# Kernel optimization log

Measured on AMD Instinct MI355X. Metric: run time of the kernel, lower is better.

## Reference

```python
import jax, jax.numpy as jnp
import numpy as np

MAX_RADIUS = 0.9
TEMP = 0.1

def _to_poincare(x, W, b):
    # Linear + Tanh, then rescale into Poincare ball of radius 0.9
    h = jnp.tanh(x @ W.T + b)
    norm = jnp.clip(jnp.linalg.norm(h, axis=-1, keepdims=True), 1e-8, None)
    scale = jnp.where(norm > MAX_RADIUS, MAX_RADIUS / norm, jnp.ones_like(norm))
    return h * scale

def setup_inputs() -> dict:
    key = jax.random.key(0)
    kq, kw, kb, km, ko = jax.random.split(key, 5)
    B, N, D = 2048, 100000, 128
    return {
        "query": jax.random.normal(kq, (B, D), dtype=jnp.float32),
        "W": jax.random.normal(kw, (D, D), dtype=jnp.float32) * (1.0 / np.sqrt(D)),
        "b": jax.random.normal(kb, (D,), dtype=jnp.float32) * 0.01,
        "mem_emb": jax.random.normal(km, (N, D), dtype=jnp.float32),
        "mem_out": jax.random.normal(ko, (N, D), dtype=jnp.float32),
        "k": 16,
    }

def reference(query, W, b, mem_emb, mem_out, k):
    q = _to_poincare(query, W, b)          # [B, D]
    m = _to_poincare(mem_emb, W, b)        # [N, D]
    # Euclidean cdist via the GEMM form: ||q||^2 + ||m||^2 - 2 q.m
    q2 = jnp.sum(q * q, axis=-1, keepdims=True)           # [B, 1]
    m2 = jnp.sum(m * m, axis=-1)                          # [N]
    d2 = q2 + m2[None, :] - 2.0 * (q @ m.T)               # [B, N]
    dists = jnp.sqrt(jnp.maximum(d2, 1e-12))
    # k smallest distances
    neg_top, top_idx = jax.lax.top_k(-dists, k)           # [B, k]
    top_dists = -neg_top
    weights = jax.nn.softmax(-top_dists / TEMP, axis=-1)  # [B, k]
    outcomes = mem_out[top_idx]                           # [B, k, D]
    return weights, outcomes
```

## Files before the change

### kernel.cpp

```cpp
#include <hip/hip_runtime.h>
#include <hip/hip_bf16.h>
#include <math.h>

#define DIM 128
#define QB 128
#define MB 64
#define NSPLIT 32
#define KSEL 16
#define KOWN 4
#define RESCORE 32
#define IDXMASK 0x1FFFu
#define KEYMASK 0xFFFFE000u
#define M2MAX 3200

using bf16x8 = __attribute__((ext_vector_type(8))) short;
using f32x4  = __attribute__((ext_vector_type(4))) float;

__device__ inline unsigned short f2bf(float f) {
  __hip_bfloat16 h = __float2bfloat16(f);
  return __builtin_bit_cast(unsigned short, h);
}
__device__ inline unsigned uminu(unsigned a, unsigned b) {
  return __builtin_elementwise_min(a, b);
}
__device__ inline unsigned umaxu(unsigned a, unsigned b) {
  return __builtin_elementwise_max(a, b);
}
__device__ inline unsigned long long umin64(unsigned long long a,
                                            unsigned long long b) {
  return __builtin_elementwise_min(a, b);
}

__device__ inline f32x4 mfma16(bf16x8 a, bf16x8 b, f32x4 c) {
  return __builtin_amdgcn_mfma_f32_16x16x32_bf16(a, b, c, 0, 0, 0);
}

__device__ inline void gload_lds16(const void* g, void* l) {
  __builtin_amdgcn_global_load_lds(
      (const __attribute__((address_space(1))) void*)g,
      (__attribute__((address_space(3))) void*)l, 16, 0, 0);
}

__device__ inline void ins4(unsigned (&ks)[KOWN], unsigned c) {
  #pragma unroll
  for (int i = 0; i < KOWN; ++i) {
    const unsigned lo = uminu(c, ks[i]);
    c = umaxu(c, ks[i]);
    ks[i] = lo;
  }
}

__global__ __launch_bounds__(512) void poincare2_k(
    const float* __restrict__ Xm, int Rm,
    const float* __restrict__ Xq, int Rq,
    const float* __restrict__ W, const float* __restrict__ bias,
    float* __restrict__ Pm, float* __restrict__ Pm2,
    float* __restrict__ Pm2s, int npadm,
    unsigned short* __restrict__ Pmbf,
    float* __restrict__ Pq, float* __restrict__ Pq2, int nbm)
{
  __shared__ float Xl[128 * DIM];
  __shared__ float nrm[128 * 8];
  __shared__ float norm2l[128];

  const int t  = threadIdx.x;
  const int l  = t & 63;
  const int wv_ = t >> 6;
  const int jw = __builtin_amdgcn_readfirstlane(wv_ * 16);

  const bool ismem = (int)blockIdx.x < nbm;
  const float* X = ismem ? Xm : Xq;
  const int    R = ismem ? Rm : Rq;
  float*       P  = ismem ? Pm  : Pq;
  float*       P2 = ismem ? Pm2 : Pq2;
  unsigned short* Pbf = ismem ? Pmbf : nullptr;
  const int rbase = (ismem ? blockIdx.x : (blockIdx.x - nbm)) * 128;

  for (int i = t; i < 128 * 32; i += 512) {
    const int r = i >> 5, c = i & 31;
    int row = rbase + r; if (row > R - 1) row = R - 1;
    const float4 v = *(const float4*)&X[(size_t)row * DIM + c * 4];
    *(float4*)&Xl[r * DIM + ((c ^ ((r >> 1) & 7)) << 2)] = v;
  }

  float acc0[16], acc1[16];
  #pragma unroll
  for (int u = 0; u < 16; ++u) {
    const float b = bias[jw + u];
    acc0[u] = b; acc1[u] = b;
  }
  __syncthreads();

  const float* Wb = W + jw * DIM;
  const int x0 = (2 * l) * DIM;
  const int x1 = x0 + DIM;
  #pragma unroll 2
  for (int k4 = 0; k4 < 32; ++k4) {
    const int ch = (k4 ^ (l & 7)) << 2;
    const float4 xv0 = *(const float4*)&Xl[x0 + ch];
    const float4 xv1 = *(const float4*)&Xl[x1 + ch];
    #pragma unroll
    for (int u = 0; u < 16; ++u) {
      const float4 wvv = *(const float4*)(Wb + u * DIM + k4 * 4);
      acc0[u] = fmaf(xv0.x, wvv.x, acc0[u]);
      acc0[u] = fmaf(xv0.y, wvv.y, acc0[u]);
      acc0[u] = fmaf(xv0.z, wvv.z, acc0[u]);
      acc0[u] = fmaf(xv0.w, wvv.w, acc0[u]);
      acc1[u] = fmaf(xv1.x, wvv.x, acc1[u]);
      acc1[u] = fmaf(xv1.y, wvv.y, acc1[u]);
      acc1[u] = fmaf(xv1.z, wvv.z, acc1[u]);
      acc1[u] = fmaf(xv1.w, wvv.w, acc1[u]);
    }
  }

  float pn0 = 0.f, pn1 = 0.f;
  #pragma unroll
  for (int u = 0; u < 16; ++u) {
    acc0[u] = tanhf(acc0[u]); pn0 = fmaf(acc0[u], acc0[u], pn0);
    acc1[u] = tanhf(acc1[u]); pn1 = fmaf(acc1[u], acc1[u], pn1);
  }
  __syncthreads();
  {
    const int cb = jw >> 2;
    #pragma unroll
    for (int u4 = 0; u4 < 4; ++u4) {
      const int pos = ((cb + u4) ^ (l & 7)) << 2;
      *(float4*)&Xl[x0 + pos] = make_float4(acc0[u4*4], acc0[u4*4+1],
                                            acc0[u4*4+2], acc0[u4*4+3]);
      *(float4*)&Xl[x1 + pos] = make_float4(acc1[u4*4], acc1[u4*4+1],
                                            acc1[u4*4+2], acc1[u4*4+3]);
    }
    nrm[(2 * l) * 8 + wv_]     = pn0;
    nrm[(2 * l + 1) * 8 + wv_] = pn1;
  }
  __syncthreads();
  if (t < 128) {
    float s = 0.f;
    #pragma unroll
    for (int j = 0; j < 8; ++j) s += nrm[t * 8 + j];
    norm2l[t] = s;
    const int row = rbase + t;
    if (row < R) {
      const float nm = sqrtf(s);
      const float sc = (nm > 0.9f) ? (0.9f / nm) : 1.0f;
      const float p2v = s * sc * sc;
      P2[row] = p2v;
      if (ismem) Pm2s[row] = fmaf(0.5f, p2v, 1.0f);
    } else if (ismem && row < npadm) {
      Pm2s[row] = __int_as_float(0x7f800000);
    }
  }
  __syncthreads();

  const int cg = t & 15, rg = t >> 4;
  #pragma unroll
  for (int v = 0; v < 4; ++v) {
    const int r = rg + 32 * v;
    const int row = rbase + r;
    if (row < R) {
      const float n2 = norm2l[r];
      const float nm = sqrtf(n2);
      const float sc = (nm > 0.9f) ? (0.9f / nm) : 1.0f;
      const int sw = (r >> 1) & 7;
      const float4 h0 = *(const float4*)&Xl[r * DIM + (((2*cg)   ^ sw) << 2)];
      const float4 h1 = *(const float4*)&Xl[r * DIM + (((2*cg+1) ^ sw) << 2)];
      float o[8] = {h0.x*sc, h0.y*sc, h0.z*sc, h0.w*sc,
                    h1.x*sc, h1.y*sc, h1.z*sc, h1.w*sc};
      *(float4*)&P[(size_t)row * DIM + cg * 8]     = make_float4(o[0], o[1], o[2], o[3]);
      *(float4*)&P[(size_t)row * DIM + cg * 8 + 4] = make_float4(o[4], o[5], o[6], o[7]);
      if (Pbf) {
        uint4 pb;
        pb.x = (unsigned)f2bf(o[0]) | ((unsigned)f2bf(o[1]) << 16);
        pb.y = (unsigned)f2bf(o[2]) | ((unsigned)f2bf(o[3]) << 16);
        pb.z = (unsigned)f2bf(o[4]) | ((unsigned)f2bf(o[5]) << 16);
        pb.w = (unsigned)f2bf(o[6]) | ((unsigned)f2bf(o[7]) << 16);
        *(uint4*)&Pmbf[(size_t)row * DIM + ((cg ^ (row & 15)) << 3)] = pb;
      }
    }
  }
}

template<bool USEBF>
__global__ __launch_bounds__(512, 2) void score_topk_k(
    const float* __restrict__ Pq,
    const float* __restrict__ Pm, const float* __restrict__ Pm2s,
    const unsigned short* __restrict__ Pmbf,
    int N, int splitlen, unsigned* __restrict__ splitTop)
{
  __shared__ __align__(16) unsigned short Ml[3][MB * DIM];
  __shared__ float m2all[M2MAX];

  const int t = threadIdx.x;
  const int lane = t & 63;
  const int w = t >> 6, wr = w >> 1, wc = w & 1;
  const int split = blockIdx.x;
  const int qbase = blockIdx.y * QB;
  const int mlo = split * splitlen;
  const int mhi = min(mlo + splitlen, N);
  const int ntiles = (mhi - mlo + MB - 1) / MB;

  bf16x8 qf[2][4];
  #pragma unroll
  for (int s = 0; s < 2; ++s) {
    const int qrow = qbase + wr * 32 + s * 16 + (lane & 15);
    #pragma unroll
    for (int ks = 0; ks < 4; ++ks) {
      const float* src = &Pq[(size_t)qrow * DIM + ks * 32 + (lane >> 4) * 8];
      float4 lo = *(const float4*)src;
      float4 hi = *(const float4*)(src + 4);
      bf16x8 v;
      v[0] = (short)f2bf(-lo.x); v[1] = (short)f2bf(-lo.y);
      v[2] = (short)f2bf(-lo.z); v[3] = (short)f2bf(-lo.w);
      v[4] = (short)f2bf(-hi.x); v[5] = (short)f2bf(-hi.y);
      v[6] = (short)f2bf(-hi.z); v[7] = (short)f2bf(-hi.w);
      qf[s][ks] = v;
    }
  }

  for (int i = t; i < splitlen; i += 512) m2all[i] = Pm2s[mlo + i];

  const size_t soff0 = (size_t)(w * 8 + (lane >> 4)) * DIM + ((lane & 15) << 3);
  const size_t soff1 = soff0 + 4 * DIM;

  auto stageU = [&](int tilei, int buf) {
    const unsigned short* b = Pmbf + (size_t)(mlo + tilei * MB) * DIM;
    gload_lds16(b + soff0, &Ml[buf][(w * 8) * DIM]);
    gload_lds16(b + soff1, &Ml[buf][(w * 8 + 4) * DIM]);
  };
  uint4 sv0, sv1;
  auto stageF_load = [&](int tilei) {
    const int fr = t >> 3, fe = t & 7;
    const float* src = Pm + (size_t)(mlo + tilei * MB + fr) * DIM + fe * 16;
    float4 a0 = *(const float4*)(src + 0);
    float4 a1 = *(const float4*)(src + 4);
    float4 a2 = *(const float4*)(src + 8);
    float4 a3 = *(const float4*)(src + 12);
    sv0.x = (unsigned)f2bf(a0.x) | ((unsigned)f2bf(a0.y) << 16);
    sv0.y = (unsigned)f2bf(a0.z) | ((unsigned)f2bf(a0.w) << 16);
    sv0.z = (unsigned)f2bf(a1.x) | ((unsigned)f2bf(a1.y) << 16);
    sv0.w = (unsigned)f2bf(a1.z) | ((unsigned)f2bf(a1.w) << 16);
    sv1.x = (unsigned)f2bf(a2.x) | ((unsigned)f2bf(a2.y) << 16);
    sv1.y = (unsigned)f2bf(a2.z) | ((unsigned)f2bf(a2.w) << 16);
    sv1.z = (unsigned)f2bf(a3.x) | ((unsigned)f2bf(a3.y) << 16);
    sv1.w = (unsigned)f2bf(a3.z) | ((unsigned)f2bf(a3.w) << 16);
  };
  auto stageF_write = [&](int buf) {
    const int fr = t >> 3, fe = t & 7;
    char* base = (char*)&Ml[buf][0] + fr * 256;
    *(uint4*)(base + (((2 * fe)     ^ (fr & 15)) << 4)) = sv0;
    *(uint4*)(base + (((2 * fe + 1) ^ (fr & 15)) << 4)) = sv1;
  };

  unsigned keys[2][4][KOWN];
  #pragma unroll
  for (int s = 0; s < 2; ++s)
    #pragma unroll
    for (int r = 0; r < 4; ++r)
      #pragma unroll
      for (int i = 0; i < KOWN; ++i) keys[s][r][i] = 0xFFFFFFFFu;

  const int mcol = wc * 32 + (lane & 15);
  const int rowA = mcol, rowB = mcol + 16;

  auto compute = [&](int tile, const unsigned short* cur) {
    const float ca = m2all[tile * MB + mcol];
    const float cb = m2all[tile * MB + mcol + 16];
    f32x4 a00 = (f32x4){ca, ca, ca, ca};
    f32x4 a01 = (f32x4){cb, cb, cb, cb};
    f32x4 a10 = (f32x4){ca, ca, ca, ca};
    f32x4 a11 = (f32x4){cb, cb, cb, cb};
    __builtin_amdgcn_s_setprio(1);
    #pragma unroll
    for (int ks = 0; ks < 4; ++ks) {
      const int kb = ks * 64 + (lane >> 4) * 16;
      bf16x8 bfrA = *(const bf16x8*)((const char*)cur + rowA * 256 +
                                     (kb ^ ((rowA & 15) << 4)));
      bf16x8 bfrB = *(const bf16x8*)((const char*)cur + rowB * 256 +
                                     (kb ^ ((rowB & 15) << 4)));
      a00 = mfma16(qf[0][ks], bfrA, a00);
      a01 = mfma16(qf[0][ks], bfrB, a01);
      a10 = mfma16(qf[1][ks], bfrA, a10);
      a11 = mfma16(qf[1][ks], bfrB, a11);
    }
    __builtin_amdgcn_s_setprio(0);
    const unsigned idx0 = (unsigned)(tile * MB + mcol);
    #pragma unroll
    for (int r = 0; r < 4; ++r) {
      ins4(keys[0][r], (__float_as_uint(a00[r]) & KEYMASK) | idx0);
      ins4(keys[0][r], (__float_as_uint(a01[r]) & KEYMASK) | (idx0 + 16));
      ins4(keys[1][r], (__float_as_uint(a10[r]) & KEYMASK) | idx0);
      ins4(keys[1][r], (__float_as_uint(a11[r]) & KEYMASK) | (idx0 + 16));
    }
  };

  if constexpr (USEBF) {
    __syncthreads();
    stageU(0, 0);
    if (ntiles > 1) stageU(1, 1);
    int cur = 0;
    for (int i = 0; i < ntiles; ++i) {
      if (i < ntiles - 1) asm volatile("s_waitcnt vmcnt(2)" ::: "memory");
      else                asm volatile("s_waitcnt vmcnt(0)" ::: "memory");
      __builtin_amdgcn_s_barrier();
      __builtin_amdgcn_sched_barrier(0);
      int nb = cur + 2; if (nb >= 3) nb -= 3;
      if (i + 2 < ntiles) stageU(i + 2, nb);
      compute(i, &Ml[cur][0]);
      cur = (cur + 1 == 3) ? 0 : cur + 1;
    }
  } else {
    stageF_load(0);
    stageF_write(0);
    __syncthreads();
    for (int i = 0; i < ntiles; ++i) {
      const int cur = i & 1;
      const bool more = (i + 1 < ntiles);
      if (more) stageF_load(i + 1);
      compute(i, &Ml[cur][0]);
      __syncthreads();
      if (more) stageF_write(cur ^ 1);
      __syncthreads();
    }
  }

  unsigned* mb = (unsigned*)&Ml[0][0];
  __syncthreads();
  #pragma unroll
  for (int s = 0; s < 2; ++s)
    #pragma unroll
    for (int r = 0; r < 4; ++r) {
      unsigned k0 = keys[s][r][0], k1 = keys[s][r][1];
      unsigned k2 = keys[s][r][2], k3 = keys[s][r][3];
      unsigned out = 0xFFFFFFFFu;
      for (int round = 0; round < 8; ++round) {
        unsigned g = k0;
        g = uminu(g, __shfl_xor(g, 1, 16));
        g = uminu(g, __shfl_xor(g, 2, 16));
        g = uminu(g, __shfl_xor(g, 4, 16));
        g = uminu(g, __shfl_xor(g, 8, 16));
        const bool mine = (k0 == g);
        k0 = mine ? k1 : k0;
        k1 = mine ? k2 : k1;
        k2 = mine ? k3 : k2;
        k3 = mine ? 0xFFFFFFFFu : k3;
        if ((lane & 15) == round) out = g;
      }
      const int lq = wr * 32 + s * 16 + (lane >> 4) * 4 + r;
      if ((lane & 15) < 8) mb[lq * 16 + wc * 8 + (lane & 15)] = out;
    }
  __syncthreads();
  if (wc == 0 && lane < 32) {
    const int lq = wr * 32 + lane;
    unsigned s8[8];
    #pragma unroll
    for (int i = 0; i < 8; ++i) s8[i] = 0xFFFFFFFFu;
    const unsigned* src = mb + lq * 16;
    #pragma unroll
    for (int i = 0; i < 16; ++i) {
      unsigned c = src[i];
      #pragma unroll
      for (int j = 0; j < 8; ++j) {
        const unsigned lo = uminu(c, s8[j]);
        c = umaxu(c, s8[j]);
        s8[j] = lo;
      }
    }
    unsigned* dst = &splitTop[((size_t)(qbase + lq) * NSPLIT + split) * 8];
    *(uint4*)dst       = make_uint4(s8[0], s8[1], s8[2], s8[3]);
    *((uint4*)dst + 1) = make_uint4(s8[4], s8[5], s8[6], s8[7]);
  }
}

__global__ __launch_bounds__(256) void finalize_k(
    const unsigned* __restrict__ splitTop,
    const float* __restrict__ Pq, const float* __restrict__ Pq2,
    const float* __restrict__ Pm, const float* __restrict__ Pm2,
    const float* __restrict__ memOut, int N, int splitlen,
    float* __restrict__ outW, float* __restrict__ outO)
{
  const int wv   = threadIdx.x >> 6;
  const int lane = threadIdx.x & 63;
  const int q = blockIdx.x * 4 + wv;

  __shared__ unsigned      sKey[4][RESCORE];
  __shared__ unsigned char sSrc[4][RESCORE];
  __shared__ unsigned long long sKeyx[4][RESCORE];
  __shared__ unsigned long long sSel[4][KSEL];
  __shared__ float sEl[4][KSEL];

  {
    unsigned a[8];
    if (lane < NSPLIT) {
      const unsigned* gp = splitTop + (size_t)q * (NSPLIT * 8) + lane * 8;
      uint4 lo = *(const uint4*)gp;
      uint4 hi = *(const uint4*)(gp + 4);
      a[0] = lo.x; a[1] = lo.y; a[2] = lo.z; a[3] = lo.w;
      a[4] = hi.x; a[5] = hi.y; a[6] = hi.z; a[7] = hi.w;
    } else {
      #pragma unroll
      for (int i = 0; i < 8; ++i) a[i] = 0xFFFFFFFFu;
    }
    for (int r = 0; r < RESCORE; ++r) {
      unsigned g = a[0];
      g = uminu(g, __shfl_xor(g, 1));
      g = uminu(g, __shfl_xor(g, 2));
      g = uminu(g, __shfl_xor(g, 4));
      g = uminu(g, __shfl_xor(g, 8));
      g = uminu(g, __shfl_xor(g, 16));
      g = uminu(g, __shfl_xor(g, 32));
      unsigned long long mask = __ballot(a[0] == g);
      const int fl = __ffsll((unsigned long long)mask) - 1;
      if (lane == fl) {
        #pragma unroll
        for (int i = 0; i < 7; ++i) a[i] = a[i + 1];
        a[7] = 0xFFFFFFFFu;
      }
      if (lane == 0) { sKey[wv][r] = g; sSrc[wv][r] = (unsigned char)fl; }
    }
  }

  #pragma unroll
  for (int p = 0; p < 4; ++p) {
    const int g8 = p * 8 + (lane >> 3), e = lane & 7;
    const int gidx = (int)sSrc[wv][g8] * splitlen + (int)(sKey[wv][g8] & IDXMASK);
    const float4* qr = (const float4*)&Pq[(size_t)q * DIM];
    const float4* mr = (const float4*)&Pm[(size_t)gidx * DIM];
    float s = 0.f;
    #pragma unroll
    for (int u = 0; u < 4; ++u) {
      float4 a = qr[e * 4 + u], b = mr[e * 4 + u];
      s = fmaf(a.x, b.x, s); s = fmaf(a.y, b.y, s);
      s = fmaf(a.z, b.z, s); s = fmaf(a.w, b.w, s);
    }
    s += __shfl_xor(s, 1, 8);
    s += __shfl_xor(s, 2, 8);
    s += __shfl_xor(s, 4, 8);
    if (e == 0) {
      float d2 = (Pq2[q] + Pm2[gidx]) - 2.0f * s;
      float dist = sqrtf(fmaxf(d2, 1e-12f));
      sKeyx[wv][g8] =
          (((unsigned long long)__float_as_uint(dist)) << 32) | (unsigned)gidx;
    }
  }

  {
    unsigned long long kk = (lane < RESCORE) ? sKeyx[wv][lane] : ~0ull;
    for (int r = 0; r < KSEL; ++r) {
      unsigned long long g = kk;
      g = umin64(g, __shfl_xor(g, 1));
      g = umin64(g, __shfl_xor(g, 2));
      g = umin64(g, __shfl_xor(g, 4));
      g = umin64(g, __shfl_xor(g, 8));
      g = umin64(g, __shfl_xor(g, 16));
      g = umin64(g, __shfl_xor(g, 32));
      if (kk == g) kk = ~0ull;
      if (lane == 0) sSel[wv][r] = g;
    }
  }

  if (lane < KSEL) {
    const float d  = __uint_as_float((unsigned)(sSel[wv][lane] >> 32));
    const float d0 = __uint_as_float((unsigned)(sSel[wv][0] >> 32));
    sEl[wv][lane] = expf((d0 - d) * 10.0f);
  }
  if (lane < KSEL) {
    float sum = 0.f;
    #pragma unroll
    for (int i = 0; i < KSEL; ++i) sum += sEl[wv][i];
    outW[(size_t)q * KSEL + lane] = sEl[wv][lane] / sum;
  }

  #pragma unroll
  for (int i = 0; i < 8; ++i) {
    const int f4 = lane + i * 64;
    const int r = f4 >> 5, c4 = f4 & 31;
    const int idx = (int)(sSel[wv][r] & 0xffffffffu);
    *(float4*)&outO[((size_t)q * KSEL + r) * DIM + c4 * 4] =
        *(const float4*)&memOut[(size_t)idx * DIM + c4 * 4];
  }
}

extern "C" void kernel_launch(void* const* d_in, const int* in_sizes, int n_in,
                              void* d_out, int out_size, void* d_ws, size_t ws_size,
                              hipStream_t stream)
{
  const float* query   = (const float*)d_in[0];
  const float* W       = (const float*)d_in[1];
  const float* bias    = (const float*)d_in[2];
  const float* mem_emb = (const float*)d_in[3];
  const float* mem_out = (const float*)d_in[4];
  const int B = in_sizes[0] / DIM;
  const int N = in_sizes[3] / DIM;

  const int splitlen = ((N + NSPLIT * MB - 1) / (NSPLIT * MB)) * MB;
  const int N_pad2 = NSPLIT * splitlen;

  float* ws  = (float*)d_ws;
  float* Pm  = ws;
  float* Pm2 = Pm + (size_t)N * DIM;
  float* Pm2s = Pm2 + N;
  float* Pq  = Pm2s + N_pad2;
  float* Pq2 = Pq + (size_t)B * DIM;
  unsigned* splitTop = (unsigned*)(Pq2 + B);
  unsigned short* Pmbf = (unsigned short*)(splitTop + (size_t)B * NSPLIT * 8);
  const size_t need_bf = (size_t)((char*)(Pmbf + (size_t)N_pad2 * DIM) - (char*)d_ws);
  const bool usebf = ws_size >= need_bf;

  float* outW = (float*)d_out;
  float* outO = outW + (size_t)B * KSEL;

  const int nbm = (N_pad2 + 127) / 128;
  const int nbq = (B + 127) / 128;
  poincare2_k<<<dim3(nbm + nbq), dim3(512), 0, stream>>>(
      mem_emb, N, query, B, W, bias, Pm, Pm2, Pm2s, N_pad2,
      usebf ? Pmbf : nullptr, Pq, Pq2, nbm);

  dim3 grid2(NSPLIT, B / QB);
  if (usebf)
    score_topk_k<true><<<grid2, dim3(512), 0, stream>>>(Pq, Pm, Pm2s, Pmbf, N,
                                                        splitlen, splitTop);
  else
    score_topk_k<false><<<grid2, dim3(512), 0, stream>>>(Pq, Pm, Pm2s, nullptr, N,
                                                         splitlen, splitTop);

  finalize_k<<<dim3(B / 4), dim3(256), 0, stream>>>(splitTop, Pq, Pq2, Pm, Pm2,
                                                    mem_out, N, splitlen,
                                                    outW, outO);
}
```

Baseline: 221.9 us.

## Drop LDS staging in projection kernel; read inputs and write outputs from registers

The Poincare projection kernel no longer stages the 128x128 input tile and the tanh results through a 64KB shared-memory buffer. Each thread now reads its two input rows straight from global memory and writes its 16-column slice of the scaled fp32 and bf16 outputs directly from registers. This removes two barriers and a large LDS footprint, which could allow more blocks per CU. The cost is uncoalesced, strided per-thread global reads and narrower scattered stores.

```diff
diff --git a/kernel.cpp b/kernel.cpp
--- a/kernel.cpp
+++ b/kernel.cpp
@@ -59,7 +59,6 @@
     unsigned short* __restrict__ Pmbf,
     float* __restrict__ Pq, float* __restrict__ Pq2, int nbm)
 {
-  __shared__ float Xl[128 * DIM];
   __shared__ float nrm[128 * 8];
   __shared__ float norm2l[128];
 
@@ -76,12 +75,10 @@
   unsigned short* Pbf = ismem ? Pmbf : nullptr;
   const int rbase = (ismem ? blockIdx.x : (blockIdx.x - nbm)) * 128;
 
-  for (int i = t; i < 128 * 32; i += 512) {
-    const int r = i >> 5, c = i & 31;
-    int row = rbase + r; if (row > R - 1) row = R - 1;
-    const float4 v = *(const float4*)&X[(size_t)row * DIM + c * 4];
-    *(float4*)&Xl[r * DIM + ((c ^ ((r >> 1) & 7)) << 2)] = v;
-  }
+  const int row0 = rbase + 2 * l;
+  const int row1 = row0 + 1;
+  const float* x0p = X + (size_t)min(row0, R - 1) * DIM;
+  const float* x1p = X + (size_t)min(row1, R - 1) * DIM;
 
   float acc0[16], acc1[16];
   #pragma unroll
@@ -89,16 +86,12 @@
     const float b = bias[jw + u];
     acc0[u] = b; acc1[u] = b;
   }
-  __syncthreads();
 
   const float* Wb = W + jw * DIM;
-  const int x0 = (2 * l) * DIM;
-  const int x1 = x0 + DIM;
-  #pragma unroll 2
+  #pragma unroll 4
   for (int k4 = 0; k4 < 32; ++k4) {
-    const int ch = (k4 ^ (l & 7)) << 2;
-    const float4 xv0 = *(const float4*)&Xl[x0 + ch];
-    const float4 xv1 = *(const float4*)&Xl[x1 + ch];
+    const float4 xv0 = *(const float4*)(x0p + k4 * 4);
+    const float4 xv1 = *(const float4*)(x1p + k4 * 4);
     #pragma unroll
     for (int u = 0; u < 16; ++u) {
       const float4 wvv = *(const float4*)(Wb + u * DIM + k4 * 4);
@@ -119,20 +112,8 @@
     acc0[u] = tanhf(acc0[u]); pn0 = fmaf(acc0[u], acc0[u], pn0);
     acc1[u] = tanhf(acc1[u]); pn1 = fmaf(acc1[u], acc1[u], pn1);
   }
-  __syncthreads();
-  {
-    const int cb = jw >> 2;
-    #pragma unroll
-    for (int u4 = 0; u4 < 4; ++u4) {
-      const int pos = ((cb + u4) ^ (l & 7)) << 2;
-      *(float4*)&Xl[x0 + pos] = make_float4(acc0[u4*4], acc0[u4*4+1],
-                                            acc0[u4*4+2], acc0[u4*4+3]);
-      *(float4*)&Xl[x1 + pos] = make_float4(acc1[u4*4], acc1[u4*4+1],
-                                            acc1[u4*4+2], acc1[u4*4+3]);
-    }
-    nrm[(2 * l) * 8 + wv_]     = pn0;
-    nrm[(2 * l + 1) * 8 + wv_] = pn1;
-  }
+  nrm[(2 * l) * 8 + wv_]     = pn0;
+  nrm[(2 * l + 1) * 8 + wv_] = pn1;
   __syncthreads();
   if (t < 128) {
     float s = 0.f;
@@ -152,29 +133,56 @@
   }
   __syncthreads();
 
-  const int cg = t & 15, rg = t >> 4;
-  #pragma unroll
-  for (int v = 0; v < 4; ++v) {
-    const int r = rg + 32 * v;
-    const int row = rbase + r;
-    if (row < R) {
-      const float n2 = norm2l[r];
+  const int g0 = jw >> 3;
+  {
+    if (row0 < R) {
+      const float n2 = norm2l[2 * l];
       const float nm = sqrtf(n2);
       const float sc = (nm > 0.9f) ? (0.9f / nm) : 1.0f;
-      const int sw = (r >> 1) & 7;
-      const float4 h0 = *(const float4*)&Xl[r * DIM + (((2*cg)   ^ sw) << 2)];
-      const float4 h1 = *(const float4*)&Xl[r * DIM + (((2*cg+1) ^ sw) << 2)];
-      float o[8] = {h0.x*sc, h0.y*sc, h0.z*sc, h0.w*sc,
-                    h1.x*sc, h1.y*sc, h1.z*sc, h1.w*sc};
-      *(float4*)&P[(size_t)row * DIM + cg * 8]     = make_float4(o[0], o[1], o[2], o[3]);
-      *(float4*)&P[(size_t)row * DIM + cg * 8 + 4] = make_float4(o[4], o[5], o[6], o[7]);
+      float o[16];
+      #pragma unroll
+      for (int u = 0; u < 16; ++u) o[u] = acc0[u] * sc;
+      #pragma unroll
+      for (int u4 = 0; u4 < 4; ++u4)
+        *(float4*)&P[(size_t)row0 * DIM + jw + u4 * 4] =
+            make_float4(o[u4*4], o[u4*4+1], o[u4*4+2], o[u4*4+3]);
       if (Pbf) {
-        uint4 pb;
-        pb.x = (unsigned)f2bf(o[0]) | ((unsigned)f2bf(o[1]) << 16);
-        pb.y = (unsigned)f2bf(o[2]) | ((unsigned)f2bf(o[3]) << 16);
-        pb.z = (unsigned)f2bf(o[4]) | ((unsigned)f2bf(o[5]) << 16);
-        pb.w = (unsigned)f2bf(o[6]) | ((unsigned)f2bf(o[7]) << 16);
-        *(uint4*)&Pmbf[(size_t)row * DIM + ((cg ^ (row & 15)) << 3)] = pb;
+        uint4 pa, pb;
+        pa.x = (unsigned)f2bf(o[0])  | ((unsigned)f2bf(o[1])  << 16);
+        pa.y = (unsigned)f2bf(o[2])  | ((unsigned)f2bf(o[3])  << 16);
+        pa.z = (unsigned)f2bf(o[4])  | ((unsigned)f2bf(o[5])  << 16);
+        pa.w = (unsigned)f2bf(o[6])  | ((unsigned)f2bf(o[7])  << 16);
+        pb.x = (unsigned)f2bf(o[8])  | ((unsigned)f2bf(o[9])  << 16);
+        pb.y = (unsigned)f2bf(o[10]) | ((unsigned)f2bf(o[11]) << 16);
+        pb.z = (unsigned)f2bf(o[12]) | ((unsigned)f2bf(o[13]) << 16);
+        pb.w = (unsigned)f2bf(o[14]) | ((unsigned)f2bf(o[15]) << 16);
+        *(uint4*)&Pmbf[(size_t)row0 * DIM + ((g0       ^ (row0 & 15)) << 3)] = pa;
+        *(uint4*)&Pmbf[(size_t)row0 * DIM + (((g0 + 1) ^ (row0 & 15)) << 3)] = pb;
+      }
+    }
+    if (row1 < R) {
+      const float n2 = norm2l[2 * l + 1];
+      const float nm = sqrtf(n2);
+      const float sc = (nm > 0.9f) ? (0.9f / nm) : 1.0f;
+      float o[16];
+      #pragma unroll
+      for (int u = 0; u < 16; ++u) o[u] = acc1[u] * sc;
+      #pragma unroll
+      for (int u4 = 0; u4 < 4; ++u4)
+        *(float4*)&P[(size_t)row1 * DIM + jw + u4 * 4] =
+            make_float4(o[u4*4], o[u4*4+1], o[u4*4+2], o[u4*4+3]);
+      if (Pbf) {
+        uint4 pa, pb;
+        pa.x = (unsigned)f2bf(o[0])  | ((unsigned)f2bf(o[1])  << 16);
+        pa.y = (unsigned)f2bf(o[2])  | ((unsigned)f2bf(o[3])  << 16);
+        pa.z = (unsigned)f2bf(o[4])  | ((unsigned)f2bf(o[5])  << 16);
+        pa.w = (unsigned)f2bf(o[6])  | ((unsigned)f2bf(o[7])  << 16);
+        pb.x = (unsigned)f2bf(o[8])  | ((unsigned)f2bf(o[9])  << 16);
+        pb.y = (unsigned)f2bf(o[10]) | ((unsigned)f2bf(o[11]) << 16);
+        pb.z = (unsigned)f2bf(o[12]) | ((unsigned)f2bf(o[13]) << 16);
+        pb.w = (unsigned)f2bf(o[14]) | ((unsigned)f2bf(o[15]) << 16);
+        *(uint4*)&Pmbf[(size_t)row1 * DIM + ((g0       ^ (row1 & 15)) << 3)] = pa;
+        *(uint4*)&Pmbf[(size_t)row1 * DIM + (((g0 + 1) ^ (row1 & 15)) << 3)] = pb;
       }
     }
   }
```

After: 250.7 us. 1.13x slower.
